# Kernel optimization log

Hardware: AMD Instinct MI355X
Metric: run time of the kernel (lower is better)

## Reference

```python
import jax, jax.numpy as jnp
import numpy as np

B, C, N = 8, 256, 4096

def setup_inputs() -> dict:
    key = jax.random.key(0)
    k1, k2, k3 = jax.random.split(key, 3)
    pts_feat = jax.random.normal(k1, (B, C, N), dtype=jnp.float32)
    # Conv1d(channels, channels, 1, bias=False) weight is [C_out, C_in, 1] -> store as [C_out, C_in]
    scale = 1.0 / np.sqrt(C)
    Wq = jax.random.uniform(k2, (C, C), dtype=jnp.float32, minval=-scale, maxval=scale)
    Wk = jax.random.uniform(k3, (C, C), dtype=jnp.float32, minval=-scale, maxval=scale)
    return {"pts_feat": pts_feat, "Wq": Wq, "Wk": Wk}

def reference(pts_feat, Wq, Wk):
    # 1x1 conv == channel-wise matmul. x_q: [B, N, C], x_k: [B, C, N]
    x_q = jnp.einsum('bcn,dc->bnd', pts_feat, Wq)
    x_k = jnp.einsum('bcn,dc->bdn', pts_feat, Wk)
    logits = jnp.einsum('bnc,bcm->bnm', x_q, x_k)          # [B, N, N]
    attn = jax.nn.softmax(logits, axis=-1)
    attn = attn / (1e-8 + attn.sum(axis=-1, keepdims=True))
    # torch.einsum('bnn,bnc->bnc', attn, feat) takes the DIAGONAL of attn
    # and scales each point's raw feature vector by it (no contraction).
    diag = jnp.diagonal(attn, axis1=1, axis2=2)            # [B, N]
    x_attn = pts_feat * diag[:, None, :]                   # [B, C, N]
    return x_attn
```

## Files before the change

kernel.cpp:

```cpp
#include <hip/hip_runtime.h>
#include <hip/hip_bf16.h>
#include <cstdint>

#define B_ 8
#define C_ 256
#define N_ 4096

typedef __bf16 bf16;
typedef __bf16 bf16x8 __attribute__((ext_vector_type(8)));
typedef float f32x4 __attribute__((ext_vector_type(4)));
typedef unsigned int u32;

__device__ __forceinline__ void async_ld16(const void* g, void* l) {
  __builtin_amdgcn_global_load_lds(
      (const __attribute__((address_space(1))) void*)g,
      (__attribute__((address_space(3))) void*)l, 16, 0, 0);
}

__device__ __forceinline__ float bh2f(unsigned short u) {
  union { u32 i; float f; } x; x.i = ((u32)u) << 16; return x.f;
}
__device__ __forceinline__ unsigned short f2bh(float f) {
  union { float f; u32 i; } x; x.f = f;
  u32 i = x.i + 0x7fffu + ((x.i >> 16) & 1u);
  return (unsigned short)(i >> 16);
}

__device__ __forceinline__ bool wave_sniff_fp32(const unsigned short* p) {
  int l = threadIdx.x & 63;
  unsigned short u = p[2 * l];
  int e = (u >> 7) & 0xff;
  unsigned long long m = __ballot(e >= 112 && e <= 142);
  return __popcll(m) < 32;
}

__global__ __launch_bounds__(256) void k_mt(const void* __restrict__ Wqv,
                                            const void* __restrict__ Wkv,
                                            unsigned short* __restrict__ Mt) {
  __shared__ float wkcol[C_];
  int t = threadIdx.x;
  bool fq = wave_sniff_fp32((const unsigned short*)Wqv);
  bool fk = wave_sniff_fp32((const unsigned short*)Wkv);
  int d = blockIdx.x, c = t;
  if (fk)
    wkcol[c] = ((const float*)Wkv)[c * C_ + d];
  else
    wkcol[c] = bh2f(((const unsigned short*)Wkv)[c * C_ + d]);
  __syncthreads();
  float acc = 0.f;
  if (fq) {
    for (int e0 = 0; e0 < C_; e0 += 16) {
      float wq[16];
#pragma unroll
      for (int j = 0; j < 16; ++j) wq[j] = ((const float*)Wqv)[(e0 + j) * C_ + c];
#pragma unroll
      for (int j = 0; j < 16; ++j) acc += wkcol[e0 + j] * wq[j];
    }
  } else {
    for (int e0 = 0; e0 < C_; e0 += 16) {
      float wq[16];
#pragma unroll
      for (int j = 0; j < 16; ++j) wq[j] = bh2f(((const unsigned short*)Wqv)[(e0 + j) * C_ + c]);
#pragma unroll
      for (int j = 0; j < 16; ++j) acc += wkcol[e0 + j] * wq[j];
    }
  }
  Mt[(size_t)d * C_ + c] = f2bh(acc * 1.44269504f);
}

__global__ __launch_bounds__(256, 2) void k_tp(const void* __restrict__ Fv,
                                               const bf16* __restrict__ Mt,
                                               unsigned short* __restrict__ Ft,
                                               bf16* __restrict__ G) {
  __shared__ unsigned short tile[128 * 70];
  __shared__ bf16 As[8 * 64 * 32];
  int n0 = blockIdx.x * 64;
  int b = blockIdx.y;
  int t = threadIdx.x;
  bool f32 = wave_sniff_fp32((const unsigned short*)Fv);

#pragma unroll
  for (int hp = 0; hp < 2; ++hp) {
    if (hp) __syncthreads();
#pragma unroll
    for (int p = 0; p < 4; ++p) {
      int cl = (t >> 3) + 32 * p;
      int n = (t & 7) * 8;
      size_t off = (size_t)(b * C_ + hp * 128 + cl) * N_ + n0 + n;
      unsigned short vals[8];
      if (f32) {
        const float* src = (const float*)Fv + off;
        float4 v0 = *(const float4*)(src);
        float4 v1 = *(const float4*)(src + 4);
        vals[0] = f2bh(v0.x); vals[1] = f2bh(v0.y); vals[2] = f2bh(v0.z); vals[3] = f2bh(v0.w);
        vals[4] = f2bh(v1.x); vals[5] = f2bh(v1.y); vals[6] = f2bh(v1.z); vals[7] = f2bh(v1.w);
      } else {
        uint4 v = *(const uint4*)((const unsigned short*)Fv + off);
        vals[0] = (unsigned short)(v.x & 0xffffu); vals[1] = (unsigned short)(v.x >> 16);
        vals[2] = (unsigned short)(v.y & 0xffffu); vals[3] = (unsigned short)(v.y >> 16);
        vals[4] = (unsigned short)(v.z & 0xffffu); vals[5] = (unsigned short)(v.z >> 16);
        vals[6] = (unsigned short)(v.w & 0xffffu); vals[7] = (unsigned short)(v.w >> 16);
      }
#pragma unroll
      for (int s = 0; s < 8; ++s) tile[cl * 70 + n + s] = vals[s];
    }
    __syncthreads();
#pragma unroll
    for (int p = 0; p < 4; ++p) {
      int idx = p * 256 + t;
      int n = idx >> 4, oc = idx & 15;
      u32 o[4];
#pragma unroll
      for (int k = 0; k < 4; ++k) {
        unsigned short lo = tile[(oc * 8 + 2 * k) * 70 + n];
        unsigned short hi = tile[(oc * 8 + 2 * k + 1) * 70 + n];
        o[k] = ((u32)hi << 16) | lo;
      }
      uint4 ov; ov.x = o[0]; ov.y = o[1]; ov.z = o[2]; ov.w = o[3];
      *(uint4*)(Ft + ((size_t)(b * N_ + n0 + n)) * C_ + hp * 128 + oc * 8) = ov;
      int gc = hp * 16 + oc;
      int kc = gc >> 2, col8 = gc & 3;
      *(uint4*)((unsigned short*)As + kc * 2048 + n * 32 + (col8 ^ ((n >> 1) & 3)) * 8) = ov;
    }
  }
  __syncthreads();

  int w = t >> 6, l = t & 63, lr = l & 15, lq = l >> 4;
  int wn = w * 32;
  int rchunk = (lq ^ ((lr >> 1) & 3)) * 8;
  const size_t fbase = (size_t)b * N_ * C_;
#pragma unroll
  for (int jp = 0; jp < 2; ++jp) {
    int d0 = jp * 128;
    bf16x8 bb[2][8];
#pragma unroll
    for (int j = 0; j < 2; ++j)
#pragma unroll
      for (int kc = 0; kc < 8; ++kc)
        bb[j][kc] = *(const bf16x8*)(Mt + (size_t)(d0 + wn + 16 * j + lr) * C_ + kc * 32 + lq * 8);
    f32x4 acc[4][2] = {};
#pragma unroll
    for (int kc = 0; kc < 8; ++kc) {
#pragma unroll
      for (int i = 0; i < 4; ++i) {
        bf16x8 a = *(const bf16x8*)(As + kc * 2048 + (16 * i + lr) * 32 + rchunk);
#pragma unroll
        for (int j = 0; j < 2; ++j)
          acc[i][j] = __builtin_amdgcn_mfma_f32_16x16x32_bf16(a, bb[j][kc], acc[i][j], 0, 0, 0);
      }
    }
    __syncthreads();
    unsigned short* Cs = (unsigned short*)tile;
#pragma unroll
    for (int i = 0; i < 4; ++i)
#pragma unroll
      for (int j = 0; j < 2; ++j)
#pragma unroll
        for (int r = 0; r < 4; ++r)
          Cs[(16 * i + lq * 4 + r) * 136 + wn + 16 * j + lr] = f2bh(acc[i][j][r]);
    __syncthreads();
#pragma unroll
    for (int p = 0; p < 4; ++p) {
      int idx = p * 256 + t;
      int row = idx >> 4, c8 = idx & 15;
      uint4 v = *(const uint4*)(Cs + row * 136 + c8 * 8);
      *(uint4*)(G + fbase + (size_t)(n0 + row) * C_ + d0 + c8 * 8) = v;
    }
  }
}

__global__ __launch_bounds__(256, 4) void k_attn(const bf16* __restrict__ G,
                                                 const bf16* __restrict__ Ft,
                                                 float* __restrict__ snn,
                                                 float* __restrict__ lsum) {
  __shared__ bf16 Ks[2][32 * 256];
  int bid = blockIdx.x;
  int b = bid & 7, q = (bid >> 3) & 3, ntile = bid >> 5;
  int n0 = ntile * 128;
  int t = threadIdx.x, w = t >> 6, l = t & 63;
  int lr = l & 15, lq = l >> 4;
  int wrow = w * 32;
  const size_t gbase = (size_t)b * N_ * C_;

  bf16x8 a[2][8];
#pragma unroll
  for (int i = 0; i < 2; ++i)
#pragma unroll
    for (int kc = 0; kc < 8; ++kc)
      a[i][kc] = *(const bf16x8*)(G + gbase + (size_t)(n0 + wrow + 16 * i + lr) * C_ + kc * 32 + lq * 8);

  float part[8];
#pragma unroll
  for (int s = 0; s < 8; ++s) part[s] = 0.f;

  int m_base = q * 1024;
  bool has_diag = (q == (ntile >> 3));
  int dbase = (ntile & 7) * 4;

  int soff[4];
#pragma unroll
  for (int p = 0; p < 4; ++p) {
    int flat = p * 256 + t;
    int kc = flat >> 7;
    int r = (flat >> 2) & 31;
    int col8 = flat & 3;
    soff[p] = r * C_ + kc * 32 + ((col8 ^ ((r >> 1) & 3)) * 8);
  }
  int rchunk = (lq ^ ((lr >> 1) & 3)) * 8;

#pragma unroll
  for (int p = 0; p < 4; ++p)
    async_ld16(Ft + gbase + (size_t)m_base * C_ + soff[p],
               (bf16*)Ks + (p * 256 + t) * 8);
  asm volatile("s_waitcnt vmcnt(0)" ::: "memory");
  __builtin_amdgcn_s_barrier();

  for (int it = 0; it < 32; ++it) {
    int cur = it & 1;
    if (it < 31) {
      int m0 = m_base + (it + 1) * 32;
#pragma unroll
      for (int p = 0; p < 4; ++p)
        async_ld16(Ft + gbase + (size_t)m0 * C_ + soff[p],
                   (bf16*)Ks + (cur ^ 1) * 8192 + (p * 256 + t) * 8);
    }
    const bf16* ks = (const bf16*)Ks + cur * 8192;
    f32x4 acc[2][2] = {};
#pragma unroll
    for (int kc = 0; kc < 8; ++kc) {
      bf16x8 b0 = *(const bf16x8*)(ks + kc * 1024 + lr * 32 + rchunk);
      bf16x8 b1 = *(const bf16x8*)(ks + kc * 1024 + (16 + lr) * 32 + rchunk);
      acc[0][0] = __builtin_amdgcn_mfma_f32_16x16x32_bf16(a[0][kc], b0, acc[0][0], 0, 0, 0);
      acc[1][0] = __builtin_amdgcn_mfma_f32_16x16x32_bf16(a[1][kc], b0, acc[1][0], 0, 0, 0);
      acc[0][1] = __builtin_amdgcn_mfma_f32_16x16x32_bf16(a[0][kc], b1, acc[0][1], 0, 0, 0);
      acc[1][1] = __builtin_amdgcn_mfma_f32_16x16x32_bf16(a[1][kc], b1, acc[1][1], 0, 0, 0);
    }
    bool dit = has_diag && ((it >> 2) == (ntile & 7));
#pragma unroll
    for (int i = 0; i < 2; ++i)
#pragma unroll
      for (int j = 0; j < 2; ++j)
#pragma unroll
        for (int r = 0; r < 4; ++r) {
          float e = __builtin_amdgcn_exp2f(acc[i][j][r]);
          part[i * 4 + r] += e;
          if (dit) {
            int rloc = wrow + 16 * i + lq * 4 + r;
            int cloc = 16 * j + lr;
            if ((it - dbase) * 32 + cloc == rloc) snn[b * N_ + n0 + rloc] = e;
          }
        }
    if (it < 31) {
      asm volatile("s_waitcnt vmcnt(0)" ::: "memory");
      __builtin_amdgcn_s_barrier();
    }
  }

#pragma unroll
  for (int s = 0; s < 8; ++s) {
    float v = part[s];
    v += __shfl_xor(v, 1);
    v += __shfl_xor(v, 2);
    v += __shfl_xor(v, 4);
    v += __shfl_xor(v, 8);
    part[s] = v;
  }
  if (lr == 0) {
#pragma unroll
    for (int i = 0; i < 2; ++i)
#pragma unroll
      for (int r = 0; r < 4; ++r)
        lsum[((size_t)q * B_ + b) * N_ + n0 + wrow + 16 * i + lq * 4 + r] = part[i * 4 + r];
  }
}

__global__ __launch_bounds__(256) void k_scale(const void* __restrict__ Fv,
                                               const float* __restrict__ snn,
                                               const float* __restrict__ lsum,
                                               void* __restrict__ Outv) {
  __shared__ __align__(16) float dd_lds[64];
  bool f32 = wave_sniff_fp32((const unsigned short*)Fv);
  int bid = blockIdx.x;
  int b = bid >> 6, n0 = (bid & 63) * 64;
  int t = threadIdx.x;
  if (t < 64) {
    int n = n0 + t;
    float s = snn[(size_t)b * N_ + n];
    float ls = 0.f;
#pragma unroll
    for (int p = 0; p < 4; ++p) ls += lsum[((size_t)p * B_ + b) * N_ + n];
    dd_lds[t] = s / (ls * (1.0f + 1e-8f));
  }
  __syncthreads();
  const size_t fb = (size_t)b * C_ * N_;
  if (f32) {
    const float* F = (const float*)Fv;
    float* O = (float*)Outv;
#pragma unroll
    for (int p = 0; p < 16; ++p) {
      int idx = p * 256 + t;
      int c = idx >> 4, ch = idx & 15;
      size_t off = fb + (size_t)c * N_ + n0 + ch * 4;
      float4 v = *(const float4*)(F + off);
      float4 d = *(const float4*)(&dd_lds[ch * 4]);
      float4 o;
      o.x = v.x * d.x; o.y = v.y * d.y; o.z = v.z * d.z; o.w = v.w * d.w;
      *(float4*)(O + off) = o;
    }
  } else {
    const unsigned short* F = (const unsigned short*)Fv;
    unsigned short* O = (unsigned short*)Outv;
#pragma unroll
    for (int p = 0; p < 8; ++p) {
      int idx = p * 256 + t;
      int c = idx >> 3, ch = idx & 7;
      size_t off = fb + (size_t)c * N_ + n0 + ch * 8;
      uint4 v = *(const uint4*)(F + off);
      u32 vv[4] = {v.x, v.y, v.z, v.w};
      u32 o[4];
#pragma unroll
      for (int k = 0; k < 4; ++k) {
        float lo = bh2f((unsigned short)(vv[k] & 0xffffu)) * dd_lds[ch * 8 + 2 * k];
        float hi = bh2f((unsigned short)(vv[k] >> 16)) * dd_lds[ch * 8 + 2 * k + 1];
        o[k] = ((u32)f2bh(hi) << 16) | f2bh(lo);
      }
      uint4 ov; ov.x = o[0]; ov.y = o[1]; ov.z = o[2]; ov.w = o[3];
      *(uint4*)(O + off) = ov;
    }
  }
}

extern "C" void kernel_launch(void* const* d_in, const int* in_sizes, int n_in,
                              void* d_out, int out_size, void* d_ws, size_t ws_size,
                              hipStream_t stream) {
  (void)in_sizes; (void)n_in; (void)out_size; (void)ws_size;
  const void* F = d_in[0];
  const void* Wq = d_in[1];
  const void* Wk = d_in[2];
  char* ws = (char*)d_ws;
  bf16* Ft = (bf16*)(ws);
  bf16* G = (bf16*)(ws + (16u << 20));
  char* tail = ws + (32u << 20);
  float* snn = (float*)(tail);
  float* lsum = (float*)(tail + 131072);
  bf16* Mt = (bf16*)(tail + 131072 + 524288);

  k_mt<<<256, 256, 0, stream>>>(Wq, Wk, (unsigned short*)Mt);
  k_tp<<<dim3(N_ / 64, B_), 256, 0, stream>>>(F, Mt, (unsigned short*)Ft, G);
  k_attn<<<1024, 256, 0, stream>>>(G, Ft, snn, lsum);
  k_scale<<<512, 256, 0, stream>>>(F, snn, lsum, d_out);
}
```

Measured before the change: 169.9 us.

## Load key tiles straight from global into registers, dropping the LDS staging

Each wave now loads its key-tile MFMA operands directly from global memory into registers, double-buffered across two register sets (bA/bB). This replaces the shared-memory async staging, which needed swizzled offsets and per-tile barriers. The goal is to remove LDS round-trips and block-wide barriers, and s_setprio is raised around the MFMA section. In exchange, every wave loads the same key tiles redundantly from global/L2, register pressure goes up with 32 extra bf16x8 vectors, and the launch-bounds occupancy hint of 4 is dropped.

```diff
diff --git a/kernel.cpp b/kernel.cpp
--- a/kernel.cpp
+++ b/kernel.cpp
@@ -169,11 +169,10 @@
   }
 }
 
-__global__ __launch_bounds__(256, 4) void k_attn(const bf16* __restrict__ G,
-                                                 const bf16* __restrict__ Ft,
-                                                 float* __restrict__ snn,
-                                                 float* __restrict__ lsum) {
-  __shared__ bf16 Ks[2][32 * 256];
+__global__ __launch_bounds__(256) void k_attn(const bf16* __restrict__ G,
+                                              const bf16* __restrict__ Ft,
+                                              float* __restrict__ snn,
+                                              float* __restrict__ lsum) {
   int bid = blockIdx.x;
   int b = bid & 7, q = (bid >> 3) & 3, ntile = bid >> 5;
   int n0 = ntile * 128;
@@ -196,65 +195,57 @@
   int m_base = q * 1024;
   bool has_diag = (q == (ntile >> 3));
   int dbase = (ntile & 7) * 4;
-
-  int soff[4];
-#pragma unroll
-  for (int p = 0; p < 4; ++p) {
-    int flat = p * 256 + t;
-    int kc = flat >> 7;
-    int r = (flat >> 2) & 31;
-    int col8 = flat & 3;
-    soff[p] = r * C_ + kc * 32 + ((col8 ^ ((r >> 1) & 3)) * 8);
-  }
-  int rchunk = (lq ^ ((lr >> 1) & 3)) * 8;
-
-#pragma unroll
-  for (int p = 0; p < 4; ++p)
-    async_ld16(Ft + gbase + (size_t)m_base * C_ + soff[p],
-               (bf16*)Ks + (p * 256 + t) * 8);
-  asm volatile("s_waitcnt vmcnt(0)" ::: "memory");
-  __builtin_amdgcn_s_barrier();
-
-  for (int it = 0; it < 32; ++it) {
-    int cur = it & 1;
-    if (it < 31) {
-      int m0 = m_base + (it + 1) * 32;
-#pragma unroll
-      for (int p = 0; p < 4; ++p)
-        async_ld16(Ft + gbase + (size_t)m0 * C_ + soff[p],
-                   (bf16*)Ks + (cur ^ 1) * 8192 + (p * 256 + t) * 8);
-    }
-    const bf16* ks = (const bf16*)Ks + cur * 8192;
-    f32x4 acc[2][2] = {};
-#pragma unroll
-    for (int kc = 0; kc < 8; ++kc) {
-      bf16x8 b0 = *(const bf16x8*)(ks + kc * 1024 + lr * 32 + rchunk);
-      bf16x8 b1 = *(const bf16x8*)(ks + kc * 1024 + (16 + lr) * 32 + rchunk);
-      acc[0][0] = __builtin_amdgcn_mfma_f32_16x16x32_bf16(a[0][kc], b0, acc[0][0], 0, 0, 0);
-      acc[1][0] = __builtin_amdgcn_mfma_f32_16x16x32_bf16(a[1][kc], b0, acc[1][0], 0, 0, 0);
-      acc[0][1] = __builtin_amdgcn_mfma_f32_16x16x32_bf16(a[0][kc], b1, acc[0][1], 0, 0, 0);
-      acc[1][1] = __builtin_amdgcn_mfma_f32_16x16x32_bf16(a[1][kc], b1, acc[1][1], 0, 0, 0);
-    }
-    bool dit = has_diag && ((it >> 2) == (ntile & 7));
-#pragma unroll
-    for (int i = 0; i < 2; ++i)
-#pragma unroll
-      for (int j = 0; j < 2; ++j)
-#pragma unroll
-        for (int r = 0; r < 4; ++r) {
-          float e = __builtin_amdgcn_exp2f(acc[i][j][r]);
-          part[i * 4 + r] += e;
-          if (dit) {
-            int rloc = wrow + 16 * i + lq * 4 + r;
-            int cloc = 16 * j + lr;
-            if ((it - dbase) * 32 + cloc == rloc) snn[b * N_ + n0 + rloc] = e;
-          }
-        }
-    if (it < 31) {
-      asm volatile("s_waitcnt vmcnt(0)" ::: "memory");
-      __builtin_amdgcn_s_barrier();
-    }
-  }
+  const bf16* fp = Ft + gbase + lr * C_ + lq * 8;
+
+  bf16x8 bA[16], bB[16];
+
+#define LOADT(bb, m0)                                                          \
+  do {                                                                         \
+    const bf16* p0_ = fp + (size_t)(m0) * C_;                                  \
+    const bf16* p1_ = p0_ + 16 * C_;                                           \
+    _Pragma("unroll") for (int kc = 0; kc < 8; ++kc) {                         \
+      bb[2 * kc] = *(const bf16x8*)(p0_ + kc * 32);                            \
+      bb[2 * kc + 1] = *(const bf16x8*)(p1_ + kc * 32);                        \
+    }                                                                          \
+  } while (0)
+
+#define EXPS(av, i, j, it)                                                     \
+  _Pragma("unroll") for (int r = 0; r < 4; ++r) {                              \
+    float e = __builtin_amdgcn_exp2f(av[r]);                                   \
+    part[(i)*4 + r] += e;                                                      \
+    if (dit) {                                                                 \
+      int rloc = wrow + 16 * (i) + lq * 4 + r;                                 \
+      int cloc = 16 * (j) + lr;                                                \
+      if (((it)-dbase) * 32 + cloc == rloc) snn[b * N_ + n0 + rloc] = e;       \
+    }                                                                          \
+  }
+
+#define COMPUTE(bb, it)                                                        \
+  do {                                                                         \
+    f32x4 a00 = {}, a01 = {}, a10 = {}, a11 = {};                              \
+    __builtin_amdgcn_s_setprio(1);                                             \
+    _Pragma("unroll") for (int kc = 0; kc < 8; ++kc) {                         \
+      a00 = __builtin_amdgcn_mfma_f32_16x16x32_bf16(a[0][kc], bb[2 * kc], a00, 0, 0, 0);     \
+      a10 = __builtin_amdgcn_mfma_f32_16x16x32_bf16(a[1][kc], bb[2 * kc], a10, 0, 0, 0);     \
+      a01 = __builtin_amdgcn_mfma_f32_16x16x32_bf16(a[0][kc], bb[2 * kc + 1], a01, 0, 0, 0); \
+      a11 = __builtin_amdgcn_mfma_f32_16x16x32_bf16(a[1][kc], bb[2 * kc + 1], a11, 0, 0, 0); \
+    }                                                                          \
+    __builtin_amdgcn_s_setprio(0);                                             \
+    bool dit = has_diag && (((it) >> 2) == (ntile & 7));                       \
+    EXPS(a00, 0, 0, it); EXPS(a01, 0, 1, it);                                  \
+    EXPS(a10, 1, 0, it); EXPS(a11, 1, 1, it);                                  \
+  } while (0)
+
+  LOADT(bA, m_base);
+  for (int itb = 0; itb < 32; itb += 2) {
+    LOADT(bB, m_base + (itb + 1) * 32);
+    COMPUTE(bA, itb);
+    if (itb < 30) LOADT(bA, m_base + (itb + 2) * 32);
+    COMPUTE(bB, itb + 1);
+  }
+#undef LOADT
+#undef EXPS
+#undef COMPUTE
 
 #pragma unroll
   for (int s = 0; s < 8; ++s) {
```

Result: slower. 341.9 us (+101.2%).
